# Performance work log

Hardware: AMD Instinct MI355X
Metric: run time of the kernel (lower is better)

The kernel has to match this reference:

```python
import jax, jax.numpy as jnp
import numpy as np

NUM_PIECES = 32

def _conv(x, w, pad):
    # NCHW conv, stride 1
    return jax.lax.conv_general_dilated(x, w, (1, 1), [(pad, pad), (pad, pad)],
                                        dimension_numbers=('NCHW', 'OIHW', 'NCHW'))

def _bn(x, s, b):
    # eval-mode BatchNorm folded to per-channel affine (running mean/var folded into s,b)
    return x * s[None, :, None, None] + b[None, :, None, None]

def setup_inputs() -> dict:
    key = jax.random.key(0)
    ks = jax.random.split(key, 24)
    N, CIN, H, W = 1024, 13, 8, 8
    C = 64          # final conv channels
    S, NB = 7, 7    # stages, conv blocks per stage
    P = NUM_PIECES
    feat = jax.random.normal(ks[0], (N, CIN - 1, H, W), jnp.float32)
    ids = jax.random.randint(ks[1], (N, 1, H, W), 0, P + 1).astype(jnp.float32)
    x = jnp.concatenate([feat, ids], axis=1)  # last channel = piece ids
    n = jax.random.normal
    inp = {
        'x': x,
        'first_w': n(ks[2], (C - 1, CIN - 1, 7, 7), jnp.float32) * 0.05,
        'first_s': 1.0 + 0.1 * n(ks[3], (C - 1,), jnp.float32),
        'first_b': 0.05 * n(ks[4], (C - 1,), jnp.float32),
        'res_w': n(ks[5], (S, NB, C, C, 7, 7), jnp.float32) * 0.02,
        'res_s': 1.0 + 0.1 * n(ks[6], (S, NB, C), jnp.float32),
        'res_b': 0.05 * n(ks[7], (S, NB, C), jnp.float32),
        'last_w': n(ks[8], (S, C, C), jnp.float32) * 0.05,
        'last_s': 1.0 + 0.1 * n(ks[9], (S, C), jnp.float32),
        'last_b': 0.05 * n(ks[10], (S, C), jnp.float32),
        'pfc1_w': n(ks[11], (256, P * C), jnp.float32) * 0.02,
        'pfc1_b': jnp.zeros((256,), jnp.float32),
        'pfc2_w': n(ks[12], (1700, 256), jnp.float32) * 0.02,
        'pfc2_b': jnp.zeros((1700,), jnp.float32),
        'vconv_w': n(ks[13], (1, C, 1, 1), jnp.float32) * 0.05,
        'v_s': 1.0 + 0.1 * n(ks[14], (1,), jnp.float32),
        'v_b': 0.05 * n(ks[15], (1,), jnp.float32),
        'vfc1_w': n(ks[16], (256, H * W), jnp.float32) * 0.02,
        'vfc1_b': jnp.zeros((256,), jnp.float32),
        'vfc2_w': n(ks[17], (1, 256), jnp.float32) * 0.02,
        'vfc2_b': jnp.zeros((1,), jnp.float32),
    }
    return inp

def reference(x, first_w, first_s, first_b, res_w, res_s, res_b, last_w, last_s, last_b,
              pfc1_w, pfc1_b, pfc2_w, pfc2_b, vconv_w, v_s, v_b,
              vfc1_w, vfc1_b, vfc2_w, vfc2_b):
    N = x.shape[0]
    P = NUM_PIECES
    conv_in = x[:, :-1]           # (N, 12, 8, 8)
    ids_f = x[:, -1]              # (N, 8, 8) float piece ids
    ids = ids_f.astype(jnp.int32)
    h = jax.nn.relu(_bn(_conv(conv_in, first_w, 3), first_s, first_b))  # (N, 63, 8, 8)
    conv_feat = jnp.concatenate([h, ids_f[:, None]], axis=1)            # (N, 64, 8, 8)
    # --- fused piece-vector extraction (replaces batch x piece torch.where loop) ---
    ids_flat = ids.reshape(N, -1)                                       # (N, 64)
    match = ids_flat[:, None, :] == jnp.arange(1, P + 1, dtype=jnp.int32)[None, :, None]  # (N,P,64)
    idx = jnp.argmax(match, axis=-1)                                    # first occurrence, row-major
    present = match.any(-1)
    board_t = conv_feat.reshape(N, conv_feat.shape[1], -1).transpose(0, 2, 1)  # (N, 64pos, C)
    piece_vec = jnp.take_along_axis(board_t, idx[:, :, None], axis=1)          # (N, P, C)
    piece_vec = piece_vec * present[:, :, None].astype(piece_vec.dtype)
    pid_hist = [piece_vec[:, :, -1][:, None, :]]
    S, NB = res_w.shape[0], res_w.shape[1]
    for i in range(S):
        h = conv_feat
        for j in range(NB):
            h = jax.nn.relu(_bn(_conv(h, res_w[i, j], 3), res_s[i, j], res_b[i, j]))
        h = _bn(jnp.einsum('nchw,oc->nohw', h, last_w[i]), last_s[i], last_b[i])  # 1x1 conv
        conv_feat = jax.nn.relu(h + conv_feat)
        pid_hist.append(piece_vec[:, :, -1][:, None, :])
    piece_ids_out = jnp.concatenate(pid_hist, axis=1)  # (N, S+1, P)
    # policy head
    hid = jax.nn.relu(piece_vec.reshape(N, -1) @ pfc1_w.T + pfc1_b)
    policy = hid @ pfc2_w.T + pfc2_b                   # (N, 1700)
    # value head
    v = jax.nn.relu(_bn(_conv(conv_feat, vconv_w, 0), v_s, v_b)).reshape(N, -1)  # (N, 64)
    v = jax.nn.relu(v @ vfc1_w.T + vfc1_b)
    value = jnp.tanh(v @ vfc2_w.T + vfc2_b)            # (N, 1)
    return (policy, value, piece_ids_out)
```

## Files before the change

### kernel.cpp

```cpp
#include <hip/hip_runtime.h>

typedef __attribute__((ext_vector_type(8)))  short          bf16x8;
typedef __attribute__((ext_vector_type(16))) float          f32x16;
typedef __attribute__((ext_vector_type(8)))  unsigned int   u32x8;
typedef __attribute__((ext_vector_type(4)))  unsigned short ushort4v;
typedef __attribute__((ext_vector_type(4)))  float          float4v;

#define DEV static __device__ __forceinline__
#define MFMA32(A,B,C) __builtin_amdgcn_mfma_f32_32x32x16_bf16(A,B,C,0,0,0)

#define NTILES   2408
#define WRES_OFF 0u
#define FW_OFF   9863168u
#define P1_OFF   9913344u
#define P2_OFF   10437632u
#define ACT0_OFF 10896384u
#define PV_OFF   15090688u
#define HID_OFF  17187840u

#define VAL_OFF 1740800
#define PID_OFF 1741824

#define ACT_A    0
#define ACT_B    32768
#define SM_Z     65536
#define SM_BYTES 65792

DEV float bf2f(unsigned short u){ union { unsigned int i; float f; } v; v.i = ((unsigned int)u) << 16; return v.f; }
DEV unsigned short f2bf(float f){
  union { float f; unsigned int i; } v; v.f = f;
  unsigned int x = v.i;
  return (unsigned short)((x + 0x7fffu + ((x >> 16) & 1u)) >> 16);
}

__global__ void prep_res_k(const float* __restrict__ res_w, unsigned short* __restrict__ ws){
  __shared__ float buf[3136];
  int bx = blockIdx.x;
  int L = bx >> 6, o = bx & 63;
  const float* src = res_w + (size_t)bx * 3136;
  for (int e = threadIdx.x; e < 3136; e += 256) buf[e] = src[e];
  __syncthreads();
  unsigned short* dst = ws + WRES_OFF;
  int mt = o >> 5, lrow = o & 31;
  int tilebase = L*49 + L/7;
  for (int e = threadIdx.x; e < 3136; e += 256){
    int t = e >> 6, c = e & 63;
    int ks = c >> 4, hi = (c >> 3) & 1, j = c & 7;
    int lane = hi*32 + lrow;
    dst[(size_t)(tilebase + t)*4096 + ((ks*2 + mt)*64 + lane)*8 + j] = f2bf(buf[c*49 + t]);
  }
}

__global__ void prep_misc_k(const float* __restrict__ first_w, const float* __restrict__ last_w,
                            const float* __restrict__ pfc1_w, const float* __restrict__ pfc2_w,
                            unsigned short* __restrict__ ws){
  const int n_fw = 49*1024, n_lw = 28672, n_p1 = 524288, n_p2 = 458752;
  const int total = n_fw + n_lw + n_p1 + n_p2;
  for (int d = blockIdx.x*256 + threadIdx.x; d < total; d += gridDim.x*256){
    if (d < n_fw){
      int t = d >> 10, r = d & 1023;
      int mt = r >> 9, lane = (r >> 3) & 63, j = r & 7;
      int o = mt*32 + (lane & 31);
      int c = ((lane >> 5) << 3) + j;
      float v = (o < 63 && c < 12) ? first_w[(o*12 + c)*49 + t] : 0.f;
      ws[FW_OFF + d] = f2bf(v);
    } else if (d < n_fw + n_lw){
      int e = d - n_fw;
      int st = e >> 12, r = e & 4095;
      int f = r >> 9, lane = (r >> 3) & 63, j = r & 7;
      int ks = f >> 1, mt = f & 1;
      int o = mt*32 + (lane & 31);
      int c = ks*16 + ((lane >> 5) << 3) + j;
      ws[WRES_OFF + (size_t)(st*344 + 343)*4096 + r] = f2bf(last_w[st*4096 + o*64 + c]);
    } else if (d < n_fw + n_lw + n_p1){
      int e = d - n_fw - n_lw; ws[P1_OFF + e] = f2bf(pfc1_w[e]);
    } else {
      int e = d - n_fw - n_lw - n_p1;
      int row = e >> 8, k = e & 255;
      ws[P2_OFF + e] = f2bf(row < 1700 ? pfc2_w[row*256 + k] : 0.f);
    }
  }
}


#define LOADW(W, q) { \
  W[0] = *(const bf16x8*)(q); \
  W[1] = *(const bf16x8*)((q) + 1024); \
  W[2] = *(const bf16x8*)((q) + 2048); \
  W[3] = *(const bf16x8*)((q) + 3072); }

#define TAPB(W, dyc, dxc) { \
  bool v_ = ((unsigned)(py + (dyc) - 3) < 8u) && ((unsigned)(px + (dxc) - 3) < 8u); \
  int pp_ = p + ((dyc) - 3)*8 + ((dxc) - 3); \
  int b_ = v_ ? (rbase + (pp_ << 7) + (hi16 ^ ((pp_ & 7) << 4))) : zaddr; \
  c0 = MFMA32(W[0], *(const bf16x8*)(sm + b_),        c0); \
  c0 = MFMA32(W[1], *(const bf16x8*)(sm + (b_ ^ 32)), c0); \
  c0 = MFMA32(W[2], *(const bf16x8*)(sm + (b_ ^ 64)), c0); \
  c0 = MFMA32(W[3], *(const bf16x8*)(sm + (b_ ^ 96)), c0); }

#define LBAR() { asm volatile("s_waitcnt lgkmcnt(0)" ::: "memory"); \
                 __builtin_amdgcn_s_barrier(); \
                 asm volatile("" ::: "memory"); }

DEV void conv_epi(const f32x16& acc, int sub, int p, int wrow, int hi,
                  unsigned char* smp, const float* sp, const float* bp){
  int swzw = (p & 7) << 4;
  #pragma unroll
  for (int rg = 0; rg < 4; ++rg){
    int o0 = sub*32 + rg*8 + hi*4;
    unsigned short bb[4];
    #pragma unroll
    for (int e = 0; e < 4; ++e){
      float v = sp[o0+e]*acc[rg*4+e] + bp[o0+e];
      v = v > 0.f ? v : 0.f;
      bb[e] = f2bf(v);
    }
    int ob = sub*64 + rg*16 + hi*8;
    *(ushort4v*)(smp + wrow + (ob ^ swzw)) = ushort4v{bb[0],bb[1],bb[2],bb[3]};
  }
}

DEV void res_epi(const f32x16& acc, u32x8& res, int sub, int p, int wrow, int hi,
                 unsigned char* smp, const float* lsp, const float* lbp){
  int swzw = (p & 7) << 4;
  #pragma unroll
  for (int rg = 0; rg < 4; ++rg){
    int o0 = sub*32 + rg*8 + hi*4;
    unsigned short bb[4];
    #pragma unroll
    for (int e = 0; e < 4; ++e){
      unsigned pr = res[rg*2 + (e>>1)];
      float rv = bf2f((unsigned short)((e & 1) ? (pr >> 16) : (pr & 0xffffu)));
      float v = lsp[o0+e]*acc[rg*4+e] + lbp[o0+e] + rv;
      v = v > 0.f ? v : 0.f;
      bb[e] = f2bf(v);
    }
    res[rg*2]   = (unsigned)bb[0] | ((unsigned)bb[1] << 16);
    res[rg*2+1] = (unsigned)bb[2] | ((unsigned)bb[3] << 16);
    int ob = sub*64 + rg*16 + hi*8;
    *(ushort4v*)(smp + wrow + (ob ^ swzw)) = ushort4v{bb[0],bb[1],bb[2],bb[3]};
  }
}

DEV void first_epi(const f32x16& acc, u32x8& res, int sub, int p, float idsv,
                   int img, int wrow, int hi, unsigned char* smp,
                   const float* fsp, const float* fbp, unsigned short* act0){
  int swzw = (p & 7) << 4;
  #pragma unroll
  for (int rg = 0; rg < 4; ++rg){
    int o0 = sub*32 + rg*8 + hi*4;
    unsigned short bb[4];
    #pragma unroll
    for (int e = 0; e < 4; ++e){
      int o = o0 + e;
      int oc = o < 63 ? o : 62;
      float v = fsp[oc]*acc[rg*4+e] + fbp[oc];
      v = v > 0.f ? v : 0.f;
      if (o == 63) v = idsv;
      bb[e] = f2bf(v);
    }
    res[rg*2]   = (unsigned)bb[0] | ((unsigned)bb[1] << 16);
    res[rg*2+1] = (unsigned)bb[2] | ((unsigned)bb[3] << 16);
    int ob = sub*64 + rg*16 + hi*8;
    *(ushort4v*)(smp + wrow + (ob ^ swzw)) = ushort4v{bb[0],bb[1],bb[2],bb[3]};
    *(ushort4v*)(act0 + (size_t)img*4096 + p*64 + o0) = ushort4v{bb[0],bb[1],bb[2],bb[3]};
  }
}

__global__ __launch_bounds__(1024, 4) void tower_k(
    const float* __restrict__ x,
    const float* __restrict__ first_s, const float* __restrict__ first_b,
    const float* __restrict__ res_s,   const float* __restrict__ res_b,
    const float* __restrict__ last_s,  const float* __restrict__ last_b,
    const float* __restrict__ vconv_w, const float* __restrict__ v_s, const float* __restrict__ v_b,
    const float* __restrict__ vfc1_w,  const float* __restrict__ vfc1_b,
    const float* __restrict__ vfc2_w,  const float* __restrict__ vfc2_b,
    const unsigned short* __restrict__ ws_r, unsigned short* __restrict__ act0,
    float* __restrict__ value_out)
{
  __shared__ unsigned char sm[SM_BYTES];
  int tid = threadIdx.x, lane = tid & 63, wave = tid >> 6;
  int imgi = wave & 3, sub = (wave >> 2) & 1, pg = wave >> 3;
  int img = blockIdx.x * 4 + imgi;

  for (int i = tid*16; i < SM_BYTES; i += 1024*16) *(float4v*)(sm + i) = float4v{0,0,0,0};
  __syncthreads();

  int col = lane & 31, hi = lane >> 5;
  int hi16 = hi << 4;
  int zaddr = SM_Z + hi16;
  int p  = pg*32 + col;
  int py = p >> 3, px = p & 7;

  const float* xim = x + (size_t)img * 832;
  int xinbase = ACT_B + imgi * 3584;
  if (wave < 4){
    int q = (lane >> 3)*14 + (lane & 7) + 3;
    for (int c = 0; c < 12; ++c)
      *(unsigned short*)(sm + xinbase + q*32 + c*2) = f2bf(xim[c*64 + lane]);
  }
  float idsv = xim[768 + p];
  __syncthreads();

  f32x16 f0 = {};
  const unsigned short* fw = ws_r + FW_OFF;
  int qbx = py*14 + px;
  #pragma unroll
  for (int dy = 0; dy < 7; ++dy){
    bool vy = (unsigned)(py + dy - 3) < 8u;
    int tq = (dy-3)*14;
    #pragma unroll
    for (int dx = 0; dx < 7; ++dx){
      int t = dy*7 + dx;
      bf16x8 a = *(const bf16x8*)(fw + t*1024 + sub*512 + lane*8);
      int q0 = qbx + tq + dx;
      int ba = vy ? (xinbase + q0*32 + hi16) : zaddr;
      f0 = MFMA32(a, *(const bf16x8*)(sm + ba), f0);
    }
  }
  u32x8 res0;
  first_epi(f0, res0, sub, p, idsv, img, ACT_A + imgi*8192 + (p << 7), hi, sm,
            first_s, first_b, act0);
  __syncthreads();

  int rbase = ACT_A + imgi*8192;
  int wbase = ACT_B + imgi*8192;
  const unsigned short* gw = ws_r + WRES_OFF + sub*512 + lane*8;

  for (int st = 0; st < 7; ++st){
    for (int j = 0; j < 7; ++j){
      int L = st*7 + j;
      f32x16 c0 = {};
      bf16x8 wA[4], wB[4];
      LOADW(wA, gw);
      #pragma unroll
      for (int t = 0; t < 49; ++t){
        const int dy = t / 7, dx = t % 7;
        if ((t & 1) == 0){
          if (t + 1 < 49) LOADW(wB, gw + (t+1)*4096);
          TAPB(wA, dy, dx);
        } else {
          if (t + 1 < 49) LOADW(wA, gw + (t+1)*4096);
          TAPB(wB, dy, dx);
        }
      }
      gw += 49*4096;
      conv_epi(c0, sub, p, wbase + (p << 7), hi, sm, res_s + L*64, res_b + L*64);
      LBAR();
      int tmpb = rbase; rbase = wbase; wbase = tmpb;
    }
    {
      bf16x8 wA[4];
      LOADW(wA, gw); gw += 4096;
      f32x16 d0 = {};
      int b = rbase + (p << 7) + (hi16 ^ ((p & 7) << 4));
      d0 = MFMA32(wA[0], *(const bf16x8*)(sm + b),        d0);
      d0 = MFMA32(wA[1], *(const bf16x8*)(sm + (b ^ 32)), d0);
      d0 = MFMA32(wA[2], *(const bf16x8*)(sm + (b ^ 64)), d0);
      d0 = MFMA32(wA[3], *(const bf16x8*)(sm + (b ^ 96)), d0);
      res_epi(d0, res0, sub, p, wbase + (p << 7), hi, sm, last_s + st*64, last_b + st*64);
      LBAR();
      int tmpb = rbase; rbase = wbase; wbase = tmpb;
    }
  }

  float part = 0.f;
  #pragma unroll
  for (int rg = 0; rg < 4; ++rg){
    #pragma unroll
    for (int eh = 0; eh < 2; ++eh){
      unsigned pr = res0[rg*2+eh];
      int ob = sub*32 + rg*8 + hi*4 + eh*2;
      part += bf2f((unsigned short)(pr & 0xffffu))*vconv_w[ob]
            + bf2f((unsigned short)(pr >> 16))*vconv_w[ob+1];
    }
  }
  part += __shfl_xor(part, 32);
  float* vpf = (float*)(sm + ACT_B);
  if (lane < 32) vpf[(imgi*2 + sub)*64 + pg*32 + lane] = part;
  __syncthreads();

  if (wave < 4){
    int mimg = blockIdx.x*4 + wave;
    float vs = v_s[0], vb = v_b[0];
    float sum = vpf[(wave*2)*64 + lane] + vpf[(wave*2 + 1)*64 + lane];
    float vv = vs*sum + vb; vv = vv > 0.f ? vv : 0.f;
    float* vbuf = (float*)(sm + ACT_B + 2048) + wave*64;
    vbuf[lane] = vv;
    asm volatile("s_waitcnt lgkmcnt(0)" ::: "memory");
    float hidv[4];
    #pragma unroll
    for (int it = 0; it < 4; ++it){
      int jj = it*64 + lane;
      float a = vfc1_b[jj];
      for (int k = 0; k < 64; k += 4){
        float4v vv4 = *(const float4v*)(vbuf + k);
        a += vfc1_w[jj*64+k]*vv4[0] + vfc1_w[jj*64+k+1]*vv4[1]
           + vfc1_w[jj*64+k+2]*vv4[2] + vfc1_w[jj*64+k+3]*vv4[3];
      }
      hidv[it] = a > 0.f ? a : 0.f;
    }
    float tot = 0.f;
    #pragma unroll
    for (int it = 0; it < 4; ++it) tot += hidv[it]*vfc2_w[it*64 + lane];
    #pragma unroll
    for (int off = 32; off; off >>= 1) tot += __shfl_xor(tot, off);
    if (lane == 0) value_out[mimg] = tanhf(tot + vfc2_b[0]);
  }
}

__global__ __launch_bounds__(256) void gather_k(const unsigned short* __restrict__ act0,
                                                unsigned short* __restrict__ pvec,
                                                float* __restrict__ pid_out){
  int lane = threadIdx.x & 63, wave = threadIdx.x >> 6;
  int img = blockIdx.x*4 + wave;
  const unsigned short* arow = act0 + (size_t)img*4096;
  int myid = (int)bf2f(arow[lane*64 + 63]);
  int mypos = 0, mypres = 0;
  for (int p = 0; p < 32; ++p){
    unsigned long long m = __ballot(myid == (p+1));
    if (lane == p){ mypres = (m != 0ull); mypos = mypres ? (__ffsll(m) - 1) : 0; }
  }
  if (lane < 32){
    float v = mypres ? (float)(lane+1) : 0.f;
    #pragma unroll
    for (int s = 0; s < 8; ++s) pid_out[(size_t)img*256 + s*32 + lane] = v;
  }
  for (int p = 0; p < 32; ++p){
    int q  = __shfl(mypos, p);
    int pr = __shfl(mypres, p);
    unsigned short v = pr ? arow[q*64 + lane] : (unsigned short)0;
    pvec[(size_t)img*2048 + p*64 + lane] = v;
  }
}

__global__ __launch_bounds__(256) void fc1_k(const unsigned short* __restrict__ pvec,
                                             const unsigned short* __restrict__ w,
                                             const float* __restrict__ bias,
                                             unsigned short* __restrict__ hid){
  int lane = threadIdx.x & 63, wave = threadIdx.x >> 6;
  int col = lane & 31, hi = lane >> 5;
  int wm = wave >> 1, wn = wave & 1;
  int m0 = blockIdx.x*128 + wm*64;
  int n0 = blockIdx.y*128 + wn*64;
  f32x16 a00 = {}, a01 = {}, a10 = {}, a11 = {};
  for (int k = 0; k < 2048; k += 16){
    bf16x8 A0 = *(const bf16x8*)(pvec + (size_t)(m0+col)*2048    + k + hi*8);
    bf16x8 A1 = *(const bf16x8*)(pvec + (size_t)(m0+32+col)*2048 + k + hi*8);
    bf16x8 B0 = *(const bf16x8*)(w + (size_t)(n0+col)*2048    + k + hi*8);
    bf16x8 B1 = *(const bf16x8*)(w + (size_t)(n0+32+col)*2048 + k + hi*8);
    a00 = MFMA32(A0, B0, a00); a01 = MFMA32(A0, B1, a01);
    a10 = MFMA32(A1, B0, a10); a11 = MFMA32(A1, B1, a11);
  }
  #pragma unroll
  for (int mt = 0; mt < 2; ++mt)
    #pragma unroll
    for (int nt = 0; nt < 2; ++nt){
      const f32x16& acc = mt == 0 ? (nt == 0 ? a00 : a01) : (nt == 0 ? a10 : a11);
      int jcol = n0 + nt*32 + col;
      float bj = bias[jcol];
      #pragma unroll
      for (int rg = 0; rg < 4; ++rg)
        #pragma unroll
        for (int e = 0; e < 4; ++e){
          int n = m0 + mt*32 + rg*8 + hi*4 + e;
          float v = acc[rg*4+e] + bj; v = v > 0.f ? v : 0.f;
          hid[(size_t)n*256 + jcol] = f2bf(v);
        }
    }
}

__global__ __launch_bounds__(256) void fc2_k(const unsigned short* __restrict__ hid,
                                             const unsigned short* __restrict__ w,
                                             const float* __restrict__ bias,
                                             float* __restrict__ pol){
  int lane = threadIdx.x & 63, wave = threadIdx.x >> 6;
  int col = lane & 31, hi = lane >> 5;
  int wm = wave >> 1, wn = wave & 1;
  int m0 = blockIdx.x*128 + wm*64;
  int n0 = blockIdx.y*128 + wn*64;
  f32x16 a00 = {}, a01 = {}, a10 = {}, a11 = {};
  for (int k = 0; k < 256; k += 16){
    bf16x8 A0 = *(const bf16x8*)(hid + (size_t)(m0+col)*256    + k + hi*8);
    bf16x8 A1 = *(const bf16x8*)(hid + (size_t)(m0+32+col)*256 + k + hi*8);
    bf16x8 B0 = *(const bf16x8*)(w + (size_t)(n0+col)*256    + k + hi*8);
    bf16x8 B1 = *(const bf16x8*)(w + (size_t)(n0+32+col)*256 + k + hi*8);
    a00 = MFMA32(A0, B0, a00); a01 = MFMA32(A0, B1, a01);
    a10 = MFMA32(A1, B0, a10); a11 = MFMA32(A1, B1, a11);
  }
  #pragma unroll
  for (int mt = 0; mt < 2; ++mt)
    #pragma unroll
    for (int nt = 0; nt < 2; ++nt){
      const f32x16& acc = mt == 0 ? (nt == 0 ? a00 : a01) : (nt == 0 ? a10 : a11);
      int jcol = n0 + nt*32 + col;
      if (jcol < 1700){
        float bj = bias[jcol];
        #pragma unroll
        for (int rg = 0; rg < 4; ++rg)
          #pragma unroll
          for (int e = 0; e < 4; ++e){
            int n = m0 + mt*32 + rg*8 + hi*4 + e;
            pol[(size_t)n*1700 + jcol] = acc[rg*4+e] + bj;
          }
      }
    }
}

extern "C" void kernel_launch(void* const* d_in, const int* in_sizes, int n_in,
                              void* d_out, int out_size, void* d_ws, size_t ws_size,
                              hipStream_t stream){
  const float* x       = (const float*)d_in[0];
  const float* first_w = (const float*)d_in[1];
  const float* first_s = (const float*)d_in[2];
  const float* first_b = (const float*)d_in[3];
  const float* res_w   = (const float*)d_in[4];
  const float* res_s   = (const float*)d_in[5];
  const float* res_b   = (const float*)d_in[6];
  const float* last_w  = (const float*)d_in[7];
  const float* last_s  = (const float*)d_in[8];
  const float* last_b  = (const float*)d_in[9];
  const float* pfc1_w  = (const float*)d_in[10];
  const float* pfc1_b  = (const float*)d_in[11];
  const float* pfc2_w  = (const float*)d_in[12];
  const float* pfc2_b  = (const float*)d_in[13];
  const float* vconv_w = (const float*)d_in[14];
  const float* v_s     = (const float*)d_in[15];
  const float* v_b     = (const float*)d_in[16];
  const float* vfc1_w  = (const float*)d_in[17];
  const float* vfc1_b  = (const float*)d_in[18];
  const float* vfc2_w  = (const float*)d_in[19];
  const float* vfc2_b  = (const float*)d_in[20];
  unsigned short* ws = (unsigned short*)d_ws;
  float* out = (float*)d_out;

  prep_res_k <<<3136, 256, 0, stream>>>(res_w, ws);
  prep_misc_k<<<1024, 256, 0, stream>>>(first_w, last_w, pfc1_w, pfc2_w, ws);
  tower_k    <<<256, 1024, 0, stream>>>(x, first_s, first_b, res_s, res_b, last_s, last_b,
                                        vconv_w, v_s, v_b, vfc1_w, vfc1_b, vfc2_w, vfc2_b,
                                        ws, ws + ACT0_OFF, out + VAL_OFF);
  gather_k   <<<256, 256, 0, stream>>>(ws + ACT0_OFF, ws + PV_OFF, out + PID_OFF);
  fc1_k      <<<dim3(8, 2), 256, 0, stream>>>(ws + PV_OFF, ws + P1_OFF, pfc1_b, ws + HID_OFF);
  fc2_k      <<<dim3(8, 14), 256, 0, stream>>>(ws + HID_OFF, ws + P2_OFF, pfc2_b, out);
}
```

Measured before the change: 1.399 ms.

## Split conv reduction over input-channel halves across waves with LDS exchange

```diff
diff --git a/kernel.cpp b/kernel.cpp
--- a/kernel.cpp
+++ b/kernel.cpp
@@ -1,6 +1,7 @@
 #include <hip/hip_runtime.h>
 
 typedef __attribute__((ext_vector_type(8)))  short          bf16x8;
+typedef __attribute__((ext_vector_type(4)))  short          bf16x4;
 typedef __attribute__((ext_vector_type(16))) float          f32x16;
 typedef __attribute__((ext_vector_type(8)))  unsigned int   u32x8;
 typedef __attribute__((ext_vector_type(4)))  unsigned short ushort4v;
@@ -21,10 +22,13 @@
 #define VAL_OFF 1740800
 #define PID_OFF 1741824
 
+#define RS       136
+#define IMG_ACT  8704
 #define ACT_A    0
-#define ACT_B    32768
-#define SM_Z     65536
-#define SM_BYTES 65792
+#define ACT_B    34816
+#define EXCH     69632
+#define SM_Z     135168
+#define SM_BYTES 135424
 
 DEV float bf2f(unsigned short u){ union { unsigned int i; float f; } v; v.i = ((unsigned int)u) << 16; return v.f; }
 DEV unsigned short f2bf(float f){
@@ -85,29 +89,54 @@
 
 #define LOADW(W, q) { \
   W[0] = *(const bf16x8*)(q); \
-  W[1] = *(const bf16x8*)((q) + 1024); \
-  W[2] = *(const bf16x8*)((q) + 2048); \
-  W[3] = *(const bf16x8*)((q) + 3072); }
+  W[1] = *(const bf16x8*)((q) + 512); \
+  W[2] = *(const bf16x8*)((q) + 1024); \
+  W[3] = *(const bf16x8*)((q) + 1536); }
 
 #define TAPB(W, dyc, dxc) { \
   bool v_ = ((unsigned)(py + (dyc) - 3) < 8u) && ((unsigned)(px + (dxc) - 3) < 8u); \
   int pp_ = p + ((dyc) - 3)*8 + ((dxc) - 3); \
-  int b_ = v_ ? (rbase + (pp_ << 7) + (hi16 ^ ((pp_ & 7) << 4))) : zaddr; \
-  c0 = MFMA32(W[0], *(const bf16x8*)(sm + b_),        c0); \
-  c0 = MFMA32(W[1], *(const bf16x8*)(sm + (b_ ^ 32)), c0); \
-  c0 = MFMA32(W[2], *(const bf16x8*)(sm + (b_ ^ 64)), c0); \
-  c0 = MFMA32(W[3], *(const bf16x8*)(sm + (b_ ^ 96)), c0); }
+  int b_ = (v_ ? rbase + pp_*RS : SM_Z) + khb; \
+  bf16x4 l0 = *(const bf16x4*)(sm + b_); \
+  bf16x4 h0 = *(const bf16x4*)(sm + b_ + 8); \
+  bf16x4 l1 = *(const bf16x4*)(sm + b_ + 32); \
+  bf16x4 h1 = *(const bf16x4*)(sm + b_ + 40); \
+  bf16x8 B0 = __builtin_shufflevector(l0, h0, 0,1,2,3,4,5,6,7); \
+  bf16x8 B1 = __builtin_shufflevector(l1, h1, 0,1,2,3,4,5,6,7); \
+  c0 = MFMA32(W[0], B0, c0); \
+  c1 = MFMA32(W[1], B0, c1); \
+  c0 = MFMA32(W[2], B1, c0); \
+  c1 = MFMA32(W[3], B1, c1); }
 
 #define LBAR() { asm volatile("s_waitcnt lgkmcnt(0)" ::: "memory"); \
                  __builtin_amdgcn_s_barrier(); \
                  asm volatile("" ::: "memory"); }
 
-DEV void conv_epi(const f32x16& acc, int sub, int p, int wrow, int hi,
+DEV f32x16 kh_exchange(unsigned char* sm, int wave, int lane, int kh,
+                       const f32x16& c0, const f32x16& c1){
+  float4v* sl = (float4v*)(sm + EXCH + wave*4096) + lane;
+  f32x16 gv = kh ? c0 : c1;
+  sl[0]   = float4v{gv[0],gv[1],gv[2],gv[3]};
+  sl[64]  = float4v{gv[4],gv[5],gv[6],gv[7]};
+  sl[128] = float4v{gv[8],gv[9],gv[10],gv[11]};
+  sl[192] = float4v{gv[12],gv[13],gv[14],gv[15]};
+  LBAR();
+  const float4v* pl = (const float4v*)(sm + EXCH + (wave^4)*4096) + lane;
+  float4v q0 = pl[0], q1 = pl[64], q2 = pl[128], q3 = pl[192];
+  f32x16 kp = kh ? c1 : c0;
+  kp[0]+=q0[0];  kp[1]+=q0[1];  kp[2]+=q0[2];  kp[3]+=q0[3];
+  kp[4]+=q1[0];  kp[5]+=q1[1];  kp[6]+=q1[2];  kp[7]+=q1[3];
+  kp[8]+=q2[0];  kp[9]+=q2[1];  kp[10]+=q2[2]; kp[11]+=q2[3];
+  kp[12]+=q3[0]; kp[13]+=q3[1]; kp[14]+=q3[2]; kp[15]+=q3[3];
+  return kp;
+}
+
+DEV void conv_epi(const f32x16& acc, int kh, int p, int wb, int hi,
                   unsigned char* smp, const float* sp, const float* bp){
-  int swzw = (p & 7) << 4;
+  int rowb = wb + p*RS + kh*64 + hi*8;
   #pragma unroll
   for (int rg = 0; rg < 4; ++rg){
-    int o0 = sub*32 + rg*8 + hi*4;
+    int o0 = kh*32 + rg*8 + hi*4;
     unsigned short bb[4];
     #pragma unroll
     for (int e = 0; e < 4; ++e){
@@ -115,17 +144,16 @@
       v = v > 0.f ? v : 0.f;
       bb[e] = f2bf(v);
     }
-    int ob = sub*64 + rg*16 + hi*8;
-    *(ushort4v*)(smp + wrow + (ob ^ swzw)) = ushort4v{bb[0],bb[1],bb[2],bb[3]};
-  }
-}
-
-DEV void res_epi(const f32x16& acc, u32x8& res, int sub, int p, int wrow, int hi,
+    *(ushort4v*)(smp + rowb + rg*16) = ushort4v{bb[0],bb[1],bb[2],bb[3]};
+  }
+}
+
+DEV void res_epi(const f32x16& acc, u32x8& res, int kh, int p, int wb, int hi,
                  unsigned char* smp, const float* lsp, const float* lbp){
-  int swzw = (p & 7) << 4;
+  int rowb = wb + p*RS + kh*64 + hi*8;
   #pragma unroll
   for (int rg = 0; rg < 4; ++rg){
-    int o0 = sub*32 + rg*8 + hi*4;
+    int o0 = kh*32 + rg*8 + hi*4;
     unsigned short bb[4];
     #pragma unroll
     for (int e = 0; e < 4; ++e){
@@ -137,18 +165,17 @@
     }
     res[rg*2]   = (unsigned)bb[0] | ((unsigned)bb[1] << 16);
     res[rg*2+1] = (unsigned)bb[2] | ((unsigned)bb[3] << 16);
-    int ob = sub*64 + rg*16 + hi*8;
-    *(ushort4v*)(smp + wrow + (ob ^ swzw)) = ushort4v{bb[0],bb[1],bb[2],bb[3]};
-  }
-}
-
-DEV void first_epi(const f32x16& acc, u32x8& res, int sub, int p, float idsv,
-                   int img, int wrow, int hi, unsigned char* smp,
+    *(ushort4v*)(smp + rowb + rg*16) = ushort4v{bb[0],bb[1],bb[2],bb[3]};
+  }
+}
+
+DEV void first_epi(const f32x16& acc, u32x8& res, int kh, int p, float idsv,
+                   int img, int wb, int hi, unsigned char* smp,
                    const float* fsp, const float* fbp, unsigned short* act0){
-  int swzw = (p & 7) << 4;
+  int rowb = wb + p*RS + kh*64 + hi*8;
   #pragma unroll
   for (int rg = 0; rg < 4; ++rg){
-    int o0 = sub*32 + rg*8 + hi*4;
+    int o0 = kh*32 + rg*8 + hi*4;
     unsigned short bb[4];
     #pragma unroll
     for (int e = 0; e < 4; ++e){
@@ -161,8 +188,7 @@
     }
     res[rg*2]   = (unsigned)bb[0] | ((unsigned)bb[1] << 16);
     res[rg*2+1] = (unsigned)bb[2] | ((unsigned)bb[3] << 16);
-    int ob = sub*64 + rg*16 + hi*8;
-    *(ushort4v*)(smp + wrow + (ob ^ swzw)) = ushort4v{bb[0],bb[1],bb[2],bb[3]};
+    *(ushort4v*)(smp + rowb + rg*16) = ushort4v{bb[0],bb[1],bb[2],bb[3]};
     *(ushort4v*)(act0 + (size_t)img*4096 + p*64 + o0) = ushort4v{bb[0],bb[1],bb[2],bb[3]};
   }
 }
@@ -180,7 +206,7 @@
 {
   __shared__ unsigned char sm[SM_BYTES];
   int tid = threadIdx.x, lane = tid & 63, wave = tid >> 6;
-  int imgi = wave & 3, sub = (wave >> 2) & 1, pg = wave >> 3;
+  int imgi = wave & 3, kh = (wave >> 2) & 1, pg = wave >> 3;
   int img = blockIdx.x * 4 + imgi;
 
   for (int i = tid*16; i < SM_BYTES; i += 1024*16) *(float4v*)(sm + i) = float4v{0,0,0,0};
@@ -188,7 +214,7 @@
 
   int col = lane & 31, hi = lane >> 5;
   int hi16 = hi << 4;
-  int zaddr = SM_Z + hi16;
+  int khb = kh*64 + hi16;
   int p  = pg*32 + col;
   int py = p >> 3, px = p & 7;
 
@@ -212,25 +238,25 @@
     #pragma unroll
     for (int dx = 0; dx < 7; ++dx){
       int t = dy*7 + dx;
-      bf16x8 a = *(const bf16x8*)(fw + t*1024 + sub*512 + lane*8);
+      bf16x8 a = *(const bf16x8*)(fw + t*1024 + kh*512 + lane*8);
       int q0 = qbx + tq + dx;
-      int ba = vy ? (xinbase + q0*32 + hi16) : zaddr;
+      int ba = vy ? (xinbase + q0*32 + hi16) : SM_Z;
       f0 = MFMA32(a, *(const bf16x8*)(sm + ba), f0);
     }
   }
   u32x8 res0;
-  first_epi(f0, res0, sub, p, idsv, img, ACT_A + imgi*8192 + (p << 7), hi, sm,
+  first_epi(f0, res0, kh, p, idsv, img, ACT_A + imgi*IMG_ACT, hi, sm,
             first_s, first_b, act0);
-  __syncthreads();
-
-  int rbase = ACT_A + imgi*8192;
-  int wbase = ACT_B + imgi*8192;
-  const unsigned short* gw = ws_r + WRES_OFF + sub*512 + lane*8;
+  LBAR();
+
+  int rbase = ACT_A + imgi*IMG_ACT;
+  int wbase = ACT_B + imgi*IMG_ACT;
+  const unsigned short* gw = ws_r + WRES_OFF + kh*2048 + lane*8;
 
   for (int st = 0; st < 7; ++st){
     for (int j = 0; j < 7; ++j){
       int L = st*7 + j;
-      f32x16 c0 = {};
+      f32x16 c0 = {}, c1 = {};
       bf16x8 wA[4], wB[4];
       LOADW(wA, gw);
       #pragma unroll
@@ -245,20 +271,28 @@
         }
       }
       gw += 49*4096;
-      conv_epi(c0, sub, p, wbase + (p << 7), hi, sm, res_s + L*64, res_b + L*64);
+      f32x16 kp = kh_exchange(sm, wave, lane, kh, c0, c1);
+      conv_epi(kp, kh, p, wbase, hi, sm, res_s + L*64, res_b + L*64);
       LBAR();
       int tmpb = rbase; rbase = wbase; wbase = tmpb;
     }
     {
       bf16x8 wA[4];
       LOADW(wA, gw); gw += 4096;
-      f32x16 d0 = {};
-      int b = rbase + (p << 7) + (hi16 ^ ((p & 7) << 4));
-      d0 = MFMA32(wA[0], *(const bf16x8*)(sm + b),        d0);
-      d0 = MFMA32(wA[1], *(const bf16x8*)(sm + (b ^ 32)), d0);
-      d0 = MFMA32(wA[2], *(const bf16x8*)(sm + (b ^ 64)), d0);
-      d0 = MFMA32(wA[3], *(const bf16x8*)(sm + (b ^ 96)), d0);
-      res_epi(d0, res0, sub, p, wbase + (p << 7), hi, sm, last_s + st*64, last_b + st*64);
+      f32x16 c0 = {}, c1 = {};
+      int b = rbase + p*RS + khb;
+      bf16x4 l0 = *(const bf16x4*)(sm + b);
+      bf16x4 h0 = *(const bf16x4*)(sm + b + 8);
+      bf16x4 l1 = *(const bf16x4*)(sm + b + 32);
+      bf16x4 h1 = *(const bf16x4*)(sm + b + 40);
+      bf16x8 B0 = __builtin_shufflevector(l0, h0, 0,1,2,3,4,5,6,7);
+      bf16x8 B1 = __builtin_shufflevector(l1, h1, 0,1,2,3,4,5,6,7);
+      c0 = MFMA32(wA[0], B0, c0);
+      c1 = MFMA32(wA[1], B0, c1);
+      c0 = MFMA32(wA[2], B1, c0);
+      c1 = MFMA32(wA[3], B1, c1);
+      f32x16 kp = kh_exchange(sm, wave, lane, kh, c0, c1);
+      res_epi(kp, res0, kh, p, wbase, hi, sm, last_s + st*64, last_b + st*64);
       LBAR();
       int tmpb = rbase; rbase = wbase; wbase = tmpb;
     }
@@ -270,14 +304,14 @@
     #pragma unroll
     for (int eh = 0; eh < 2; ++eh){
       unsigned pr = res0[rg*2+eh];
-      int ob = sub*32 + rg*8 + hi*4 + eh*2;
+      int ob = kh*32 + rg*8 + hi*4 + eh*2;
       part += bf2f((unsigned short)(pr & 0xffffu))*vconv_w[ob]
             + bf2f((unsigned short)(pr >> 16))*vconv_w[ob+1];
     }
   }
   part += __shfl_xor(part, 32);
-  float* vpf = (float*)(sm + ACT_B);
-  if (lane < 32) vpf[(imgi*2 + sub)*64 + pg*32 + lane] = part;
+  float* vpf = (float*)(sm + EXCH);
+  if (lane < 32) vpf[(imgi*2 + kh)*64 + pg*32 + lane] = part;
   __syncthreads();
 
   if (wave < 4){
@@ -285,7 +319,7 @@
     float vs = v_s[0], vb = v_b[0];
     float sum = vpf[(wave*2)*64 + lane] + vpf[(wave*2 + 1)*64 + lane];
     float vv = vs*sum + vb; vv = vv > 0.f ? vv : 0.f;
-    float* vbuf = (float*)(sm + ACT_B + 2048) + wave*64;
+    float* vbuf = (float*)(sm + EXCH + 2048) + wave*64;
     vbuf[lane] = vv;
     asm volatile("s_waitcnt lgkmcnt(0)" ::: "memory");
     float hidv[4];
```

Result: slower. 2.483 ms (+77.5%).
